# Kernel tuning notes

Hardware: AMD Instinct MI355X
Metric: run time of the kernel (lower is better)

The kernel has to match this reference:

```python
import jax, jax.numpy as jnp
import numpy as np

N_NODES = 100000

def gcn_conv(x, W, b, row, col, n):
    # PyG GCNConv: linear transform, then D^-1/2 A_hat D^-1/2 aggregation (+bias).
    xw = x @ W                                            # [N, out]
    deg = jax.ops.segment_sum(jnp.ones_like(col, dtype=xw.dtype), col, num_segments=n)
    dinv = jnp.where(deg > 0, jax.lax.rsqrt(jnp.maximum(deg, 1e-12)), 0.0)
    norm = dinv[row] * dinv[col]                          # [E]
    msgs = xw[row] * norm[:, None]                        # gather + scale
    out = jax.ops.segment_sum(msgs, col, num_segments=n)  # scatter-add
    return out + b


def setup_inputs() -> dict:
    key = jax.random.key(0)
    k = jax.random.split(key, 9)
    n, e = N_NODES, 1600000
    d_in, d_h, d_out = 128, 64, 40
    def glorot(kk, fi, fo):
        s = jnp.sqrt(6.0 / (fi + fo))
        return jax.random.uniform(kk, (fi, fo), jnp.float32, -s, s)
    return {
        "x": jax.random.normal(k[0], (n, d_in), jnp.float32),
        "edge_index": jax.random.randint(k[1], (2, e), 0, n, jnp.int64),
        "W1": glorot(k[2], d_in, d_h), "b1": jnp.zeros((d_h,), jnp.float32),
        "W2": glorot(k[3], d_h, d_h),  "b2": jnp.zeros((d_h,), jnp.float32),
        "W3": glorot(k[4], d_h, d_out), "b3": jnp.zeros((d_out,), jnp.float32),
    }


def reference(x, edge_index, W1, b1, W2, b2, W3, b3):
    n = x.shape[0]
    loops = jnp.arange(n, dtype=edge_index.dtype)
    row = jnp.concatenate([edge_index[0], loops])  # self-loops added, as in GCNConv
    col = jnp.concatenate([edge_index[1], loops])
    h = jax.nn.relu(gcn_conv(x, W1, b1, row, col, n))
    h = jax.nn.relu(gcn_conv(h, W2, b2, row, col, n))
    return gcn_conv(h, W3, b3, row, col, n)
```

## Files before the change

kernel.cpp:

```cpp
#include <hip/hip_runtime.h>
#include <hip/hip_fp16.h>

constexpr int TPB = 256;
constexpr int SH = 9;
constexpr int BD = 1 << SH;
constexpr int CHUNK = 4096;

typedef _Float16 half8 __attribute__((ext_vector_type(8)));
typedef float float4v __attribute__((ext_vector_type(4)));

__device__ __forceinline__ int wave_incl_scan(int x, int lane) {
#pragma unroll
  for (int d = 1; d < 64; d <<= 1) {
    int y = __shfl_up(x, d);
    if (lane >= d) x += y;
  }
  return x;
}


__global__ void bin_kernel(const int* __restrict__ row, const int* __restrict__ col,
                           int* __restrict__ bcur, int2* __restrict__ binned,
                           int e, int nb, int cap) {
  __shared__ int h[512];
  __shared__ int base[512];
  for (int i = threadIdx.x; i < nb; i += TPB) h[i] = 0;
  __syncthreads();
  int cb = blockIdx.x * CHUNK;
  int lim = min(cb + CHUNK, e);
  for (int i = cb + threadIdx.x; i < lim; i += TPB)
    atomicAdd(&h[col[i] >> SH], 1);
  __syncthreads();
  for (int i = threadIdx.x; i < nb; i += TPB) {
    int c = h[i];
    base[i] = c ? (i * cap + atomicAdd(&bcur[i], c)) : 0;
    h[i] = 0;
  }
  __syncthreads();
  for (int i = cb + threadIdx.x; i < lim; i += TPB) {
    int c = col[i];
    int b = c >> SH;
    int p = base[b] + atomicAdd(&h[b], 1);
    binned[p] = make_int2(row[i], c);
  }
}

__global__ __launch_bounds__(512) void count_place_kernel(
    const int2* __restrict__ binned, const int* __restrict__ bcnt, int cap,
    int2* __restrict__ offs2, float* __restrict__ dinv, int* __restrict__ csr, int n) {
  __shared__ int cnt[BD];
  __shared__ int wsum[8];
  int t = threadIdx.x, lane = t & 63, wv = t >> 6;
  int b = blockIdx.x;
  int c0 = b << SH;
  int ndst = min(BD, n - c0);
  cnt[t] = 0;
  __syncthreads();
  int beg = b * cap;
  int end = beg + bcnt[b];
  for (int i = beg + t; i < end; i += 512)
    atomicAdd(&cnt[binned[i].y - c0], 1);
  __syncthreads();
  int v = cnt[t];
  int ps = wave_incl_scan(v, lane);
  if (lane == 63) wsum[wv] = ps;
  __syncthreads();
  int woff = 0;
#pragma unroll
  for (int w = 0; w < 8; w++) woff += (w < wv) ? wsum[w] : 0;
  int ex = woff + ps - v;
  if (t < ndst) {
    offs2[c0 + t] = make_int2(beg + ex, beg + ex + v);
    dinv[c0 + t] = rsqrtf(1.0f + (float)v);
  }
  __syncthreads();
  cnt[t] = beg + ex;
  __syncthreads();
  for (int i = beg + t; i < end; i += 512) {
    int2 rc = binned[i];
    int p = atomicAdd(&cnt[rc.y - c0], 1);
    csr[p] = rc.x;
  }
}


template <int K, int M, int CT, int KT>
__device__ __forceinline__ void pack_one(const float* __restrict__ W,
                                         _Float16* __restrict__ P, int idx) {
  if (idx >= CT * KT * 64 * 8) return;
  int j = idx & 7;
  int lane = (idx >> 3) & 63;
  int f = idx >> 9;
  int kt = f % KT, ct = f / KT;
  int c = ct * 16 + (lane & 15);
  int k = kt * 32 + (lane >> 4) * 8 + j;
  float v = (c < M) ? W[k * M + c] : 0.f;
  P[idx] = (_Float16)v;
}

__global__ __launch_bounds__(256) void pack_all_kernel(
    const float* __restrict__ W1, const float* __restrict__ W2,
    const float* __restrict__ W3, _Float16* __restrict__ P1,
    _Float16* __restrict__ P2, _Float16* __restrict__ P3, int* __restrict__ bcur) {
  int blk = blockIdx.x, t = threadIdx.x;
  if (blk < 32) {
    pack_one<128, 64, 4, 4>(W1, P1, blk * 256 + t);
  } else if (blk < 48) {
    pack_one<64, 64, 4, 2>(W2, P2, (blk - 32) * 256 + t);
  } else if (blk < 60) {
    pack_one<64, 40, 3, 2>(W3, P3, (blk - 48) * 256 + t);
  } else {
    bcur[t] = 0;
    bcur[t + 256] = 0;
  }
}


template <int K, int M, int CT>
__global__ __launch_bounds__(256) void gemm_mfma_f32in(const float* __restrict__ x,
                                                       const _Float16* __restrict__ PW,
                                                       const float* __restrict__ dinv,
                                                       _Float16* __restrict__ out, int n) {
  constexpr int KT = K / 32;
  int lane = threadIdx.x & 63, wv = threadIdx.x >> 6;
  int m = lane & 15, q = lane >> 4;
  int row0w = blockIdx.x * 64 + wv * 16;
  int arow = row0w + m;
  int ar = arow < n ? arow : n - 1;
  const half8* pw = (const half8*)PW;

  float4v acc[CT];
#pragma unroll
  for (int ct = 0; ct < CT; ct++) acc[ct] = (float4v){0.f, 0.f, 0.f, 0.f};

#pragma unroll
  for (int kt = 0; kt < KT; kt++) {
    const float* xp = x + (size_t)ar * K + kt * 32 + q * 8;
    float4 x0 = *(const float4*)xp;
    float4 x1 = *(const float4*)(xp + 4);
    half8 a;
    a[0] = (_Float16)x0.x; a[1] = (_Float16)x0.y;
    a[2] = (_Float16)x0.z; a[3] = (_Float16)x0.w;
    a[4] = (_Float16)x1.x; a[5] = (_Float16)x1.y;
    a[6] = (_Float16)x1.z; a[7] = (_Float16)x1.w;
#pragma unroll
    for (int ct = 0; ct < CT; ct++) {
      half8 b = pw[(ct * KT + kt) * 64 + lane];
      acc[ct] = __builtin_amdgcn_mfma_f32_16x16x32_f16(a, b, acc[ct], 0, 0, 0);
    }
  }
  int r0 = row0w + q * 4;
  float dv[4];
#pragma unroll
  for (int reg = 0; reg < 4; reg++) dv[reg] = (r0 + reg < n) ? dinv[r0 + reg] : 0.f;
#pragma unroll
  for (int ct = 0; ct < CT; ct++) {
    int c = ct * 16 + m;
    if (c < M) {
#pragma unroll
      for (int reg = 0; reg < 4; reg++) {
        int r = r0 + reg;
        if (r < n) out[(size_t)r * M + c] = (_Float16)(acc[ct][reg] * dv[reg]);
      }
    }
  }
}


__device__ __forceinline__ void h8_add(uint4 u, float* acc) {
  __half2 h0 = *(__half2*)&u.x, h1 = *(__half2*)&u.y;
  __half2 h2 = *(__half2*)&u.z, h3 = *(__half2*)&u.w;
  float2 f0 = __half22float2(h0), f1 = __half22float2(h1);
  float2 f2 = __half22float2(h2), f3 = __half22float2(h3);
  acc[0] += f0.x; acc[1] += f0.y; acc[2] += f1.x; acc[3] += f1.y;
  acc[4] += f2.x; acc[5] += f2.y; acc[6] += f3.x; acc[7] += f3.y;
}

__device__ __forceinline__ uint4 pack_h8(const float* o) {
  __half2 h0 = __float22half2_rn(make_float2(o[0], o[1]));
  __half2 h1 = __float22half2_rn(make_float2(o[2], o[3]));
  __half2 h2 = __float22half2_rn(make_float2(o[4], o[5]));
  __half2 h3 = __float22half2_rn(make_float2(o[6], o[7]));
  uint4 u;
  u.x = *(unsigned*)&h0;
  u.y = *(unsigned*)&h1;
  u.z = *(unsigned*)&h2;
  u.w = *(unsigned*)&h3;
  return u;
}

__device__ __forceinline__ void agg_node(const uint4* __restrict__ xw4,
                                         const int* __restrict__ csr,
                                         int beg, int end, int sb, int half,
                                         int fl, int fl16, float* acc) {
  int b = beg;
  int idx0 = b + fl16;
  int rr = (idx0 < end) ? csr[idx0] : 0;
  while (b < end) {
    int bn = b + 16;
    int idxn = bn + fl16;
    int rn = (idxn < end) ? csr[idxn] : 0;
    int cnt = end - b;
    uint4 u[8];
    int r[8];
#pragma unroll
    for (int j = 0; j < 8; j++) {
      int ej = 2 * j + half;
      r[j] = __shfl(rr, sb + ej);
    }
#pragma unroll
    for (int j = 0; j < 8; j++) {
      int ej = 2 * j + half;
      if (ej < cnt) u[j] = xw4[(size_t)r[j] * 8 + fl];
    }
#pragma unroll
    for (int j = 0; j < 8; j++) {
      int ej = 2 * j + half;
      if (ej < cnt) h8_add(u[j], acc);
    }
    rr = rn;
    b = bn;
  }
}


__global__ __launch_bounds__(256) void agg_mid_kernel(
    const uint4* __restrict__ xw4, const float* __restrict__ dinv,
    const int* __restrict__ csr, const int2* __restrict__ offs2,
    const float* __restrict__ bias, uint4* __restrict__ out4, int n) {
  int lane = threadIdx.x & 63, wv = threadIdx.x >> 6;
  int sl = lane >> 4, fl16 = lane & 15, half = fl16 >> 3, fl = fl16 & 7;
  int sb = sl << 4;
  int i = blockIdx.x * 16 + wv * 4 + sl;
  bool valid = i < n;
  int ic = valid ? i : n - 1;
  int2 oe = offs2[ic];
  int beg = oe.x;
  int end = valid ? oe.y : beg;
  float di = dinv[ic];
  float acc[8] = {0.f, 0.f, 0.f, 0.f, 0.f, 0.f, 0.f, 0.f};
  if (!half) h8_add(xw4[(size_t)ic * 8 + fl], acc);
  agg_node(xw4, csr, beg, end, sb, half, fl, fl16, acc);
#pragma unroll
  for (int k = 0; k < 8; k++) acc[k] += __shfl_xor(acc[k], 8);

  if (valid && !half) {
    const float4* b4 = (const float4*)bias;
    float4 ba = b4[fl * 2], bb = b4[fl * 2 + 1];
    float o[8];
    o[0] = fmaxf(acc[0] * di + ba.x, 0.f) * di;
    o[1] = fmaxf(acc[1] * di + ba.y, 0.f) * di;
    o[2] = fmaxf(acc[2] * di + ba.z, 0.f) * di;
    o[3] = fmaxf(acc[3] * di + ba.w, 0.f) * di;
    o[4] = fmaxf(acc[4] * di + bb.x, 0.f) * di;
    o[5] = fmaxf(acc[5] * di + bb.y, 0.f) * di;
    o[6] = fmaxf(acc[6] * di + bb.z, 0.f) * di;
    o[7] = fmaxf(acc[7] * di + bb.w, 0.f) * di;
    out4[(size_t)i * 8 + fl] = pack_h8(o);
  }
}


template <int M, int CT, int FMODE>
__global__ __launch_bounds__(256) void fused_agg_gemm(
    const uint4* __restrict__ xw4, const float* __restrict__ dinv,
    const int* __restrict__ csr, const int2* __restrict__ offs2,
    const float* __restrict__ biasA, const float* __restrict__ biasG,
    const _Float16* __restrict__ PW, void* __restrict__ outp, int n) {
  constexpr int KT = 2;
  __shared__ _Float16 tile[64 * 72];
  int lane = threadIdx.x & 63, wv = threadIdx.x >> 6;
  int sl = lane >> 4, fl16 = lane & 15, half = fl16 >> 3, fl = fl16 & 7;
  int sb = sl << 4;
  int slot_id = wv * 4 + sl;
  int base = blockIdx.x * 64;

#pragma unroll 1
  for (int nd = 0; nd < 4; nd++) {
    int l = slot_id * 4 + nd;
    int i = base + l;
    bool valid = i < n;
    int ic = valid ? i : n - 1;
    int2 oe = offs2[ic];
    int beg = oe.x;
    int end = valid ? oe.y : beg;
    float di = dinv[ic];
    float acc[8] = {0.f, 0.f, 0.f, 0.f, 0.f, 0.f, 0.f, 0.f};
    if (!half) h8_add(xw4[(size_t)ic * 8 + fl], acc);
    agg_node(xw4, csr, beg, end, sb, half, fl, fl16, acc);
#pragma unroll
    for (int k = 0; k < 8; k++) acc[k] += __shfl_xor(acc[k], 8);

    float o[8];
    if (FMODE == 0) {
      const float4* b4 = (const float4*)biasA;
      float4 ba = b4[fl * 2], bb = b4[fl * 2 + 1];
      o[0] = fmaxf(acc[0] * di + ba.x, 0.f);
      o[1] = fmaxf(acc[1] * di + ba.y, 0.f);
      o[2] = fmaxf(acc[2] * di + ba.z, 0.f);
      o[3] = fmaxf(acc[3] * di + ba.w, 0.f);
      o[4] = fmaxf(acc[4] * di + bb.x, 0.f);
      o[5] = fmaxf(acc[5] * di + bb.y, 0.f);
      o[6] = fmaxf(acc[6] * di + bb.z, 0.f);
      o[7] = fmaxf(acc[7] * di + bb.w, 0.f);
    } else {
#pragma unroll
      for (int k = 0; k < 8; k++) o[k] = acc[k] * di;
    }
    if (!half) *(uint4*)&tile[(size_t)l * 72 + fl * 8] = pack_h8(o);
  }
  __syncthreads();

  int m = lane & 15, q = lane >> 4;
  int lrow = wv * 16 + m;
  const half8* pw = (const half8*)PW;
  float4v accd[CT];
#pragma unroll
  for (int ct = 0; ct < CT; ct++) accd[ct] = (float4v){0.f, 0.f, 0.f, 0.f};
#pragma unroll
  for (int kt = 0; kt < KT; kt++) {
    half8 a = *(const half8*)&tile[lrow * 72 + kt * 32 + q * 8];
#pragma unroll
    for (int ct = 0; ct < CT; ct++) {
      half8 b = pw[(ct * KT + kt) * 64 + lane];
      accd[ct] = __builtin_amdgcn_mfma_f32_16x16x32_f16(a, b, accd[ct], 0, 0, 0);
    }
  }
  int r0 = base + wv * 16 + q * 4;
  if (FMODE == 0) {
    _Float16* out = (_Float16*)outp;
    float dv[4];
#pragma unroll
    for (int reg = 0; reg < 4; reg++) dv[reg] = (r0 + reg < n) ? dinv[r0 + reg] : 0.f;
#pragma unroll
    for (int ct = 0; ct < CT; ct++) {
      int c = ct * 16 + m;
      if (c < M) {
#pragma unroll
        for (int reg = 0; reg < 4; reg++) {
          int r = r0 + reg;
          if (r < n) out[(size_t)r * M + c] = (_Float16)(accd[ct][reg] * dv[reg]);
        }
      }
    }
  } else {
    float* out = (float*)outp;
#pragma unroll
    for (int ct = 0; ct < CT; ct++) {
      int c = ct * 16 + m;
      if (c < M) {
        float bb = biasG[c];
#pragma unroll
        for (int reg = 0; reg < 4; reg++) {
          int r = r0 + reg;
          if (r < n) out[(size_t)r * M + c] = accd[ct][reg] + bb;
        }
      }
    }
  }
}


extern "C" void kernel_launch(void* const* d_in, const int* in_sizes, int n_in,
                              void* d_out, int out_size, void* d_ws, size_t ws_size,
                              hipStream_t stream) {
  const float* x  = (const float*)d_in[0];
  const int*   ei = (const int*)d_in[1];
  const float* W1 = (const float*)d_in[2];
  const float* b1 = (const float*)d_in[3];
  const float* W2 = (const float*)d_in[4];
  const float* b2 = (const float*)d_in[5];
  const float* W3 = (const float*)d_in[6];
  const float* b3 = (const float*)d_in[7];

  int n = in_sizes[0] / 128;
  int e = in_sizes[1] / 2;
  const int* rowA = ei;
  const int* colA = ei + e;

  int nb = (n + BD - 1) >> SH;
  int meanb = e / nb;
  int cap = meanb + (meanb / 4 > 1024 ? meanb / 4 : 1024);
  int nch = (e + CHUNK - 1) / CHUNK;

  size_t off = 0;
  auto alloc = [&](size_t bytes) {
    void* p = (char*)d_ws + off;
    off += (bytes + 255) & ~(size_t)255;
    return p;
  };
  __half* bufA  = (__half*)alloc((size_t)n * 64 * 4);
  __half* bufB  = (__half*)alloc((size_t)n * 64 * 4);
  int2*  offs2  = (int2*)alloc((size_t)n * 8);
  float* dinv   = (float*)alloc((size_t)n * 4);
  int*   csr    = (int*)alloc((size_t)nb * cap * 4);
  int*   bcur   = (int*)alloc(512 * 4);
  _Float16* PW1 = (_Float16*)alloc(4 * 4 * 64 * 8 * 2);
  _Float16* PW2 = (_Float16*)alloc(4 * 2 * 64 * 8 * 2);
  _Float16* PW3 = (_Float16*)alloc(3 * 2 * 64 * 8 * 2);
  int2*  binned = (int2*)bufA;
  (void)ws_size; (void)n_in; (void)out_size;

  pack_all_kernel<<<61, TPB, 0, stream>>>(W1, W2, W3, PW1, PW2, PW3, bcur);
  bin_kernel<<<nch, TPB, 0, stream>>>(rowA, colA, bcur, binned, e, nb, cap);
  count_place_kernel<<<nb, 512, 0, stream>>>(binned, bcur, cap, offs2, dinv, csr, n);

  int gmf = (n + 63) / 64;
  int gagg = (n + 15) / 16;

  gemm_mfma_f32in<128, 64, 4><<<gmf, TPB, 0, stream>>>(x, PW1, dinv, (_Float16*)bufA, n);
  fused_agg_gemm<64, 4, 0><<<gmf, TPB, 0, stream>>>(
      (const uint4*)bufA, dinv, csr, offs2, b1, nullptr, PW2, bufB, n);
  agg_mid_kernel<<<gagg, TPB, 0, stream>>>((const uint4*)bufB, dinv, csr, offs2,
                                           b2, (uint4*)bufA, n);
  fused_agg_gemm<40, 3, 1><<<gmf, TPB, 0, stream>>>(
      (const uint4*)bufA, dinv, csr, offs2, nullptr, b3, PW3, d_out, n);
}
```

Before: 256.5 us.

## Pack binned edges into 32-bit words, shrink bins, prefetch node metadata

Binned edge records are packed into a single 32-bit word (local column in the high 9 bits, row in the low 23 bits) instead of an int2, halving the traffic of the binning and placement passes. Bin width drops from 512 to 256 destinations, which doubles the number of count_place blocks and halves the shared counters each block uses. The fused aggregation kernel now loads offsets and dinv for its four nodes up front rather than inside the serial loop. The packing assumes row indices fit in 23 bits, and the smaller bins mean more blocks, each with less work.

```diff
diff --git a/kernel.cpp b/kernel.cpp
--- a/kernel.cpp
+++ b/kernel.cpp
@@ -2,9 +2,10 @@
 #include <hip/hip_fp16.h>
 
 constexpr int TPB = 256;
-constexpr int SH = 9;
+constexpr int SH = 8;
 constexpr int BD = 1 << SH;
 constexpr int CHUNK = 4096;
+constexpr int RMASK = (1 << 23) - 1;
 
 typedef _Float16 half8 __attribute__((ext_vector_type(8)));
 typedef float float4v __attribute__((ext_vector_type(4)));
@@ -20,7 +21,7 @@
 
 
 __global__ void bin_kernel(const int* __restrict__ row, const int* __restrict__ col,
-                           int* __restrict__ bcur, int2* __restrict__ binned,
+                           int* __restrict__ bcur, int* __restrict__ binned,
                            int e, int nb, int cap) {
   __shared__ int h[512];
   __shared__ int base[512];
@@ -41,12 +42,12 @@
     int c = col[i];
     int b = c >> SH;
     int p = base[b] + atomicAdd(&h[b], 1);
-    binned[p] = make_int2(row[i], c);
+    binned[p] = ((c & (BD - 1)) << 23) | row[i];
   }
 }
 
 __global__ __launch_bounds__(512) void count_place_kernel(
-    const int2* __restrict__ binned, const int* __restrict__ bcnt, int cap,
+    const int* __restrict__ binned, const int* __restrict__ bcnt, int cap,
     int2* __restrict__ offs2, float* __restrict__ dinv, int* __restrict__ csr, int n) {
   __shared__ int cnt[BD];
   __shared__ int wsum[8];
@@ -54,14 +55,14 @@
   int b = blockIdx.x;
   int c0 = b << SH;
   int ndst = min(BD, n - c0);
-  cnt[t] = 0;
+  if (t < BD) cnt[t] = 0;
   __syncthreads();
   int beg = b * cap;
   int end = beg + bcnt[b];
   for (int i = beg + t; i < end; i += 512)
-    atomicAdd(&cnt[binned[i].y - c0], 1);
-  __syncthreads();
-  int v = cnt[t];
+    atomicAdd(&cnt[(unsigned)binned[i] >> 23], 1);
+  __syncthreads();
+  int v = (t < BD) ? cnt[t] : 0;
   int ps = wave_incl_scan(v, lane);
   if (lane == 63) wsum[wv] = ps;
   __syncthreads();
@@ -74,12 +75,12 @@
     dinv[c0 + t] = rsqrtf(1.0f + (float)v);
   }
   __syncthreads();
-  cnt[t] = beg + ex;
+  if (t < BD) cnt[t] = beg + ex;
   __syncthreads();
   for (int i = beg + t; i < end; i += 512) {
-    int2 rc = binned[i];
-    int p = atomicAdd(&cnt[rc.y - c0], 1);
-    csr[p] = rc.x;
+    int pv = binned[i];
+    int p = atomicAdd(&cnt[(unsigned)pv >> 23], 1);
+    csr[p] = pv & RMASK;
   }
 }
 
@@ -275,16 +276,26 @@
   int slot_id = wv * 4 + sl;
   int base = blockIdx.x * 64;
 
+  int ic4[4];
+  int2 oe4[4];
+  float di4[4];
+#pragma unroll
+  for (int nd = 0; nd < 4; nd++) {
+    int i = base + slot_id * 4 + nd;
+    ic4[nd] = (i < n) ? i : n - 1;
+    oe4[nd] = offs2[ic4[nd]];
+    di4[nd] = dinv[ic4[nd]];
+  }
+
 #pragma unroll 1
   for (int nd = 0; nd < 4; nd++) {
     int l = slot_id * 4 + nd;
     int i = base + l;
     bool valid = i < n;
-    int ic = valid ? i : n - 1;
-    int2 oe = offs2[ic];
-    int beg = oe.x;
-    int end = valid ? oe.y : beg;
-    float di = dinv[ic];
+    int ic = ic4[nd];
+    int beg = oe4[nd].x;
+    int end = valid ? oe4[nd].y : beg;
+    float di = di4[nd];
     float acc[8] = {0.f, 0.f, 0.f, 0.f, 0.f, 0.f, 0.f, 0.f};
     if (!half) h8_add(xw4[(size_t)ic * 8 + fl], acc);
     agg_node(xw4, csr, beg, end, sb, half, fl, fl16, acc);
@@ -398,7 +409,7 @@
   _Float16* PW1 = (_Float16*)alloc(4 * 4 * 64 * 8 * 2);
   _Float16* PW2 = (_Float16*)alloc(4 * 2 * 64 * 8 * 2);
   _Float16* PW3 = (_Float16*)alloc(3 * 2 * 64 * 8 * 2);
-  int2*  binned = (int2*)bufA;
+  int*   binned = (int*)bufA;
   (void)ws_size; (void)n_in; (void)out_size;
 
   pack_all_kernel<<<61, TPB, 0, stream>>>(W1, W2, W3, PW1, PW2, PW3, bcur);
```

Result: slower. 284.4 us (+10.9%).
